# Kernel tuning notes

Hardware: AMD Instinct MI355X
Metric: run time of the kernel (lower is better)

Reference implementation:

```python
import jax, jax.numpy as jnp
import numpy as np

N_HEADS = 16


def setup_inputs() -> dict:
    key = jax.random.key(0)
    k1, k2, k3 = jax.random.split(key, 3)
    B, T, C = 4, 2048, 1024
    x = jax.random.normal(k1, (B, T, C), dtype=jnp.float32)
    # torch nn.Linear weights are (out_features, in_features); y = x @ W.T
    w_in = jax.random.normal(k2, (3 * C, C), dtype=jnp.float32) * 0.02
    w_out = jax.random.normal(k3, (C, C), dtype=jnp.float32) * 0.02
    return {"x": x, "w_in": w_in, "w_out": w_out}


def reference(x, w_in, w_out):
    B, T, C = x.shape
    H = N_HEADS
    hd = C // H

    qkv = x @ w_in.T                      # [B, T, 3C]
    q, k, v = jnp.split(qkv, 3, axis=2)   # each [B, T, C]

    def heads(t):
        return t.reshape(B, T, H, hd).transpose(0, 2, 1, 3)  # [B, H, T, hd]

    q, k, v = heads(q), heads(k), heads(v)

    scale = 1.0 / jnp.sqrt(jnp.float32(hd))
    scores = jnp.einsum('bhqd,bhkd->bhqk', q, k) * scale      # [B, H, T, T]
    causal = jnp.tril(jnp.ones((T, T), dtype=bool))
    scores = jnp.where(causal, scores, -jnp.inf)
    attn = jax.nn.softmax(scores, axis=-1)
    y = jnp.einsum('bhqk,bhkd->bhqd', attn, v)                # [B, H, T, hd]
    y = y.transpose(0, 2, 1, 3).reshape(B, T, C)
    return y @ w_out.T
```

## Files before the change

kernel.cpp:

```cpp
#include <hip/hip_runtime.h>
#include <stdint.h>

#define BB 4
#define TT 2048
#define CC 1024
#define HH 16
#define HD 64
#define C3 3072
#define MM (BB*TT)

typedef __bf16 bf16_t;
typedef bf16_t bf16x8 __attribute__((ext_vector_type(8)));
typedef float f32x4 __attribute__((ext_vector_type(4)));
typedef unsigned short u16;
typedef u16 u16x8 __attribute__((ext_vector_type(8)));
typedef uint32_t u32;

static __device__ __forceinline__ u16 f2bf(float f){
  u32 u = __builtin_bit_cast(u32, f);
  u32 r = (u + 0x7fffu + ((u >> 16) & 1u)) >> 16;
  return (u16)r;
}

static __device__ __forceinline__ f32x4 mfma16(bf16x8 a, bf16x8 b, f32x4 c){
  return __builtin_amdgcn_mfma_f32_16x16x32_bf16(a, b, c, 0, 0, 0);
}

typedef __attribute__((address_space(1))) void* gas_t;
typedef __attribute__((address_space(3))) void* las_t;
static __device__ __forceinline__ void gload16(const void* g, void* l){
  __builtin_amdgcn_global_load_lds((gas_t)g, (las_t)l, 16, 0, 0);
}

__global__ __launch_bounds__(256) void cvt_bf16(const float* __restrict__ in,
                                                u16* __restrict__ out, int n8){
  int stride = gridDim.x * blockDim.x;
  for (int i = blockIdx.x * blockDim.x + threadIdx.x; i < n8; i += stride){
    const float4* p = (const float4*)in + (size_t)i * 2;
    float4 a = p[0], b = p[1];
    u16x8 o;
    o[0]=f2bf(a.x); o[1]=f2bf(a.y); o[2]=f2bf(a.z); o[3]=f2bf(a.w);
    o[4]=f2bf(b.x); o[5]=f2bf(b.y); o[6]=f2bf(b.z); o[7]=f2bf(b.w);
    *((u16x8*)out + i) = o;
  }
}

template<int OUTBF>
__global__ __launch_bounds__(256) void gemm_bt(const u16* __restrict__ A,
                                               const u16* __restrict__ Bm,
                                               void* __restrict__ Cp,
                                               int M, int N, int K){
  __shared__ u16 As[128*32];
  __shared__ u16 Bs[128*32];
  const int tid  = threadIdx.x;
  const int lane = tid & 63;
  const int w    = tid >> 6;
  const int m0   = blockIdx.y * 128;
  const int n0   = blockIdx.x * 128;
  const int wm   = (w >> 1) * 64;
  const int wn   = (w & 1) * 64;
  const int lr   = lane & 15;
  const int lkb  = (lane >> 4) * 16;

  f32x4 acc[4][4] = {};

  const int r0 = w*32 + (lane >> 2);
  const int c8 = (lane & 3) * 8;
  const u16* gA = A  + (size_t)(m0 + r0) * K + c8;
  const u16* gB = Bm + (size_t)(n0 + r0) * K + c8;
  char* lA = (char*)As + w*2048 + lane*16;
  char* lB = (char*)Bs + w*2048 + lane*16;

  for (int k0 = 0; k0 < K; k0 += 32){
    gload16(gA + k0,                 lA);
    gload16(gA + (size_t)16*K + k0,  lA + 1024);
    gload16(gB + k0,                 lB);
    gload16(gB + (size_t)16*K + k0,  lB + 1024);
    __syncthreads();
    bf16x8 af[4], bfr[4];
    #pragma unroll
    for (int m = 0; m < 4; m++)
      af[m] = *(const bf16x8*)((const char*)As + (wm + m*16 + lr)*64 + lkb);
    #pragma unroll
    for (int n = 0; n < 4; n++)
      bfr[n] = *(const bf16x8*)((const char*)Bs + (wn + n*16 + lr)*64 + lkb);
    #pragma unroll
    for (int m = 0; m < 4; m++)
      #pragma unroll
      for (int n = 0; n < 4; n++)
        acc[m][n] = mfma16(af[m], bfr[n], acc[m][n]);
    __syncthreads();
  }

  const int cr = (lane >> 4) * 4;
  #pragma unroll
  for (int m = 0; m < 4; m++)
    #pragma unroll
    for (int n = 0; n < 4; n++)
      #pragma unroll
      for (int j = 0; j < 4; j++){
        size_t row = (size_t)(m0 + wm + m*16 + cr + j);
        size_t col = (size_t)(n0 + wn + n*16 + lr);
        if (OUTBF) ((u16*)Cp)[row*(size_t)N + col] = f2bf(acc[m][n][j]);
        else       ((float*)Cp)[row*(size_t)N + col] = acc[m][n][j];
      }
}

__global__ __launch_bounds__(256, 2) void attn_fwd(const u16* __restrict__ qkv,
                                                   u16* __restrict__ y){
  __shared__ u16 Kl[64*72];
  __shared__ u16 Vt[64*72];
  const int bid = blockIdx.x;
  const int tq = bid >> 6;
  const int h = bid & 15, b = (bid >> 4) & 3;
  const int tid = threadIdx.x, lane = tid & 63, w = tid >> 6;
  const int lr = lane & 15, lg = lane >> 4;
  const size_t base = (size_t)b * TT * C3;
  const int qA = tq*64 + w*16;
  const int qB = (31-tq)*64 + w*16;

  bf16x8 qf[2][2];
  {
    const u16* qp0 = qkv + base + (size_t)(qA + lr) * C3 + h*HD;
    qf[0][0] = *(const bf16x8*)(qp0 + lg*8);
    qf[0][1] = *(const bf16x8*)(qp0 + 32 + lg*8);
    const u16* qp1 = qkv + base + (size_t)(qB + lr) * C3 + h*HD;
    qf[1][0] = *(const bf16x8*)(qp1 + lg*8);
    qf[1][1] = *(const bf16x8*)(qp1 + 32 + lg*8);
  }

  const int rK = tid >> 3, cK = tid & 7;
  const int rV = tid & 31, cV = tid >> 5;
  const u16* gK = qkv + base + (size_t)rK * C3 + CC   + h*HD + cK*8;
  const u16* gV = qkv + base + (size_t)rV * C3 + 2*CC + h*HD + cV*8;

  const int kkey = ((rK >> 3) & 1) << 5;
  const int kw0 = rK*72 + ((cK*8) ^ kkey);
  const int kw1 = (rK+32)*72 + ((cK*8) ^ kkey);

  const int rdx = ((lr >> 2) & 1) << 5;
  const int rbase = 8*(lr >> 2) + (lr & 3);

  u16x8 kreg[2], vreg[2];
  kreg[0] = *(const u16x8*)(gK);
  kreg[1] = *(const u16x8*)(gK + (size_t)32*C3);
  vreg[0] = *(const u16x8*)(gV);
  vreg[1] = *(const u16x8*)(gV + (size_t)32*C3);

  f32x4 o[2][4] = {};
  float mj[2] = {-1e30f, -1e30f};
  float lj[2] = {0.f, 0.f};
  const float SC = 0.18033688011112042f;

  const int ktmax = 31 - tq;
  for (int kt = 0; kt <= ktmax; kt++){
    __syncthreads();
    *(u16x8*)&Kl[kw0] = kreg[0];
    *(u16x8*)&Kl[kw1] = kreg[1];
    #pragma unroll
    for (int i = 0; i < 2; i++)
      #pragma unroll
      for (int e = 0; e < 8; e++)
        Vt[(cV*8+e)*72 + i*32 + rV] = vreg[i][e];
    __syncthreads();

    if (kt < ktmax){
      const u16* gk2 = gK + (size_t)(kt+1)*64*C3;
      const u16* gv2 = gV + (size_t)(kt+1)*64*C3;
      kreg[0] = *(const u16x8*)(gk2);
      kreg[1] = *(const u16x8*)(gk2 + (size_t)32*C3);
      vreg[0] = *(const u16x8*)(gv2);
      vreg[1] = *(const u16x8*)(gv2 + (size_t)32*C3);
    }

    const bool m0act = (kt <= tq);

    f32x4 s[2][4] = {};
    __builtin_amdgcn_s_setprio(1);
    #pragma unroll
    for (int n = 0; n < 4; n++){
      const int rho = 32*(n>>1) + 4*(n&1) + rbase;
      bf16x8 kb0 = *(const bf16x8*)&Kl[rho*72 + ((     lg*8) ^ rdx)];
      bf16x8 kb1 = *(const bf16x8*)&Kl[rho*72 + ((32 + lg*8) ^ rdx)];
      if (m0act){
        s[0][n] = mfma16(kb0, qf[0][0], s[0][n]);
        s[0][n] = mfma16(kb1, qf[0][1], s[0][n]);
      }
      s[1][n] = mfma16(kb0, qf[1][0], s[1][n]);
      s[1][n] = mfma16(kb1, qf[1][1], s[1][n]);
    }
    __builtin_amdgcn_s_setprio(0);

    bf16x8 paA[2], paB[2];
    #pragma unroll
    for (int m = 0; m < 2; m++){
      if (m == 0 && !m0act) continue;
      const int qrow = (m ? qB : qA) + lr;
      const bool dm = (kt == (m ? ktmax : tq));
      float t[4][4];
      #pragma unroll
      for (int n = 0; n < 4; n++)
        #pragma unroll
        for (int j = 0; j < 4; j++){
          float v = s[m][n][j] * SC;
          if (dm && (kt*64 + 32*(n>>1) + 8*lg + 4*(n&1) + j > qrow)) v = -1e30f;
          t[n][j] = v;
        }
      float tm = t[0][0];
      #pragma unroll
      for (int n = 0; n < 4; n++)
        #pragma unroll
        for (int j = 0; j < 4; j++) tm = fmaxf(tm, t[n][j]);
      tm = fmaxf(tm, __shfl_xor(tm, 16, 64));
      tm = fmaxf(tm, __shfl_xor(tm, 32, 64));
      float mo = mj[m];
      if (!__all(tm <= mo)){
        float mn = fmaxf(mo, tm);
        float al = __builtin_amdgcn_exp2f(mo - mn);
        mj[m] = mn;
        lj[m] *= al;
        float a0 = __shfl(al, lg*4+0, 16);
        float a1 = __shfl(al, lg*4+1, 16);
        float a2 = __shfl(al, lg*4+2, 16);
        float a3 = __shfl(al, lg*4+3, 16);
        #pragma unroll
        for (int n = 0; n < 4; n++){
          o[m][n][0] *= a0; o[m][n][1] *= a1;
          o[m][n][2] *= a2; o[m][n][3] *= a3;
        }
      }
      float mm = mj[m];
      float ps = 0.f;
      float p[4][4];
      #pragma unroll
      for (int n = 0; n < 4; n++){
        p[n][0] = __builtin_amdgcn_exp2f(t[n][0] - mm);
        p[n][1] = __builtin_amdgcn_exp2f(t[n][1] - mm);
        p[n][2] = __builtin_amdgcn_exp2f(t[n][2] - mm);
        p[n][3] = __builtin_amdgcn_exp2f(t[n][3] - mm);
        ps += (p[n][0] + p[n][1]) + (p[n][2] + p[n][3]);
      }
      ps += __shfl_xor(ps, 16, 64);
      ps += __shfl_xor(ps, 32, 64);
      lj[m] += ps;
      bf16x8 pa, pb;
      #pragma unroll
      for (int j = 0; j < 4; j++){
        pa[j]   = (bf16_t)p[0][j];
        pa[4+j] = (bf16_t)p[1][j];
        pb[j]   = (bf16_t)p[2][j];
        pb[4+j] = (bf16_t)p[3][j];
      }
      paA[m] = pa; paB[m] = pb;
    }

    __builtin_amdgcn_s_setprio(1);
    #pragma unroll
    for (int n = 0; n < 4; n++){
      bf16x8 vb0 = *(const bf16x8*)&Vt[(n*16+lr)*72 +      lg*8];
      bf16x8 vb1 = *(const bf16x8*)&Vt[(n*16+lr)*72 + 32 + lg*8];
      if (m0act){
        o[0][n] = mfma16(paA[0], vb0, o[0][n]);
        o[0][n] = mfma16(paB[0], vb1, o[0][n]);
      }
      o[1][n] = mfma16(paA[1], vb0, o[1][n]);
      o[1][n] = mfma16(paB[1], vb1, o[1][n]);
    }
    __builtin_amdgcn_s_setprio(0);
  }

  #pragma unroll
  for (int m = 0; m < 2; m++){
    float inv = 1.0f / lj[m];
    float i0 = __shfl(inv, lg*4+0, 16);
    float i1 = __shfl(inv, lg*4+1, 16);
    float i2 = __shfl(inv, lg*4+2, 16);
    float i3 = __shfl(inv, lg*4+3, 16);
    const int qb = (m ? qB : qA);
    #pragma unroll
    for (int j = 0; j < 4; j++){
      float ij = (j==0) ? i0 : (j==1) ? i1 : (j==2) ? i2 : i3;
      size_t row = (size_t)b*TT + qb + lg*4 + j;
      #pragma unroll
      for (int n = 0; n < 4; n++)
        y[row*CC + h*HD + n*16 + lr] = f2bf(o[m][n][j] * ij);
    }
  }
}

extern "C" void kernel_launch(void* const* d_in, const int* in_sizes, int n_in,
                              void* d_out, int out_size, void* d_ws, size_t ws_size,
                              hipStream_t stream){
  const float* x     = (const float*)d_in[0];
  const float* w_in  = (const float*)d_in[1];
  const float* w_out = (const float*)d_in[2];
  float* out = (float*)d_out;

  u16* xb   = (u16*)d_ws;
  u16* wib  = xb  + (size_t)MM * CC;
  u16* wob  = wib + (size_t)C3 * CC;
  u16* qkvb = wob + (size_t)CC * CC;
  u16* yb   = xb;

  auto nblk = [](int n8){ int g = (n8 + 255) / 256; return g > 2048 ? 2048 : g; };
  cvt_bf16<<<nblk(MM*CC/8), 256, 0, stream>>>(x,     xb,  MM*CC/8);
  cvt_bf16<<<nblk(C3*CC/8), 256, 0, stream>>>(w_in,  wib, C3*CC/8);
  cvt_bf16<<<nblk(CC*CC/8), 256, 0, stream>>>(w_out, wob, CC*CC/8);

  gemm_bt<1><<<dim3(C3/128, MM/128), 256, 0, stream>>>(xb, wib, (void*)qkvb, MM, C3, CC);
  attn_fwd<<<1024, 256, 0, stream>>>(qkvb, yb);
  gemm_bt<0><<<dim3(CC/128, MM/128), 256, 0, stream>>>(yb, wob, (void*)out, MM, CC, CC);
}
```

Baseline: 197.3 us.

## Deepen GEMM K-tile with swizzled LDS, remap blocks per XCD, streamline softmax

The GEMM now loads 64-wide K tiles into an XOR-swizzled shared-memory layout, which halves barrier count and reduces LDS bank conflicts. It also remaps the 1D block id so that consecutive tiles land on the same XCD for L2 reuse. In attention, the softmax scale is folded into Q once at load, the mask is applied in place, and the max rescale is skipped unless the new max exceeds the old by more than 4. Occupancy is raised to 3 blocks per SM. Risks include register spills at the higher occupancy, extra Q rounding, and the lazy rescale threshold allowing larger exponent values.

```diff
diff --git a/kernel.cpp b/kernel.cpp
--- a/kernel.cpp
+++ b/kernel.cpp
@@ -49,50 +49,64 @@
 __global__ __launch_bounds__(256) void gemm_bt(const u16* __restrict__ A,
                                                const u16* __restrict__ Bm,
                                                void* __restrict__ Cp,
-                                               int M, int N, int K){
-  __shared__ u16 As[128*32];
-  __shared__ u16 Bs[128*32];
+                                               int M, int N, int K,
+                                               int nbx, int cpx){
+  __shared__ u16 As[128*64];
+  __shared__ u16 Bs[128*64];
+  const int bid = blockIdx.x;
+  const int nb = (bid & 7) * cpx + (bid >> 3);
+  const int by = nb / nbx, bx = nb - by * nbx;
   const int tid  = threadIdx.x;
   const int lane = tid & 63;
   const int w    = tid >> 6;
-  const int m0   = blockIdx.y * 128;
-  const int n0   = blockIdx.x * 128;
+  const int m0   = by * 128;
+  const int n0   = bx * 128;
   const int wm   = (w >> 1) * 64;
   const int wn   = (w & 1) * 64;
   const int lr   = lane & 15;
-  const int lkb  = (lane >> 4) * 16;
+  const int lg4  = lane >> 4;
 
   f32x4 acc[4][4] = {};
 
-  const int r0 = w*32 + (lane >> 2);
-  const int c8 = (lane & 3) * 8;
-  const u16* gA = A  + (size_t)(m0 + r0) * K + c8;
-  const u16* gB = Bm + (size_t)(n0 + r0) * K + c8;
-  char* lA = (char*)As + w*2048 + lane*16;
-  char* lB = (char*)Bs + w*2048 + lane*16;
-
-  for (int k0 = 0; k0 < K; k0 += 32){
-    gload16(gA + k0,                 lA);
-    gload16(gA + (size_t)16*K + k0,  lA + 1024);
-    gload16(gB + k0,                 lB);
-    gload16(gB + (size_t)16*K + k0,  lB + 1024);
+  const int rq  = tid >> 3;
+  const int c8s = ((tid & 7) ^ (rq & 7)) * 8;
+  const u16* gA = A  + (size_t)(m0 + rq) * K + c8s;
+  const u16* gB = Bm + (size_t)(n0 + rq) * K + c8s;
+  char* lA = (char*)As + tid*16;
+  char* lB = (char*)Bs + tid*16;
+
+  for (int k0 = 0; k0 < K; k0 += 64){
+    #pragma unroll
+    for (int q = 0; q < 4; q++){
+      gload16(gA + (size_t)(q*32)*K + k0, lA + q*4096);
+      gload16(gB + (size_t)(q*32)*K + k0, lB + q*4096);
+    }
     __syncthreads();
-    bf16x8 af[4], bfr[4];
-    #pragma unroll
-    for (int m = 0; m < 4; m++)
-      af[m] = *(const bf16x8*)((const char*)As + (wm + m*16 + lr)*64 + lkb);
-    #pragma unroll
-    for (int n = 0; n < 4; n++)
-      bfr[n] = *(const bf16x8*)((const char*)Bs + (wn + n*16 + lr)*64 + lkb);
-    #pragma unroll
-    for (int m = 0; m < 4; m++)
-      #pragma unroll
-      for (int n = 0; n < 4; n++)
-        acc[m][n] = mfma16(af[m], bfr[n], acc[m][n]);
+    #pragma unroll
+    for (int kk = 0; kk < 2; kk++){
+      bf16x8 af[4], bfr[4];
+      #pragma unroll
+      for (int m = 0; m < 4; m++){
+        int row = wm + m*16 + lr;
+        int slot = ((kk<<2) | lg4) ^ (row & 7);
+        af[m] = *(const bf16x8*)((const char*)As + row*128 + slot*16);
+      }
+      #pragma unroll
+      for (int n = 0; n < 4; n++){
+        int row = wn + n*16 + lr;
+        int slot = ((kk<<2) | lg4) ^ (row & 7);
+        bfr[n] = *(const bf16x8*)((const char*)Bs + row*128 + slot*16);
+      }
+      #pragma unroll
+      for (int m = 0; m < 4; m++)
+        #pragma unroll
+        for (int n = 0; n < 4; n++)
+          acc[m][n] = mfma16(af[m], bfr[n], acc[m][n]);
+    }
     __syncthreads();
   }
 
-  const int cr = (lane >> 4) * 4;
+  const int cr = lg4 * 4;
   #pragma unroll
   for (int m = 0; m < 4; m++)
     #pragma unroll
@@ -106,7 +120,7 @@
       }
 }
 
-__global__ __launch_bounds__(256, 2) void attn_fwd(const u16* __restrict__ qkv,
+__global__ __launch_bounds__(256, 3) void attn_fwd(const u16* __restrict__ qkv,
                                                    u16* __restrict__ y){
   __shared__ u16 Kl[64*72];
   __shared__ u16 Vt[64*72];
@@ -118,6 +132,7 @@
   const size_t base = (size_t)b * TT * C3;
   const int qA = tq*64 + w*16;
   const int qB = (31-tq)*64 + w*16;
+  const float SC = 0.18033688011112042f;
 
   bf16x8 qf[2][2];
   {
@@ -127,6 +142,13 @@
     const u16* qp1 = qkv + base + (size_t)(qB + lr) * C3 + h*HD;
     qf[1][0] = *(const bf16x8*)(qp1 + lg*8);
     qf[1][1] = *(const bf16x8*)(qp1 + 32 + lg*8);
+    #pragma unroll
+    for (int m = 0; m < 2; m++)
+      #pragma unroll
+      for (int i = 0; i < 2; i++)
+        #pragma unroll
+        for (int e = 0; e < 8; e++)
+          qf[m][i][e] = (bf16_t)((float)qf[m][i][e] * SC);
   }
 
   const int rK = tid >> 3, cK = tid & 7;
@@ -150,7 +172,6 @@
   f32x4 o[2][4] = {};
   float mj[2] = {-1e30f, -1e30f};
   float lj[2] = {0.f, 0.f};
-  const float SC = 0.18033688011112042f;
 
   const int ktmax = 31 - tq;
   for (int kt = 0; kt <= ktmax; kt++){
@@ -197,24 +218,23 @@
       if (m == 0 && !m0act) continue;
       const int qrow = (m ? qB : qA) + lr;
       const bool dm = (kt == (m ? ktmax : tq));
-      float t[4][4];
+      if (dm){
+        #pragma unroll
+        for (int n = 0; n < 4; n++)
+          #pragma unroll
+          for (int j = 0; j < 4; j++)
+            if (kt*64 + 32*(n>>1) + 8*lg + 4*(n&1) + j > qrow)
+              s[m][n][j] = -1e30f;
+      }
+      float tm = s[m][0][0];
       #pragma unroll
       for (int n = 0; n < 4; n++)
         #pragma unroll
-        for (int j = 0; j < 4; j++){
-          float v = s[m][n][j] * SC;
-          if (dm && (kt*64 + 32*(n>>1) + 8*lg + 4*(n&1) + j > qrow)) v = -1e30f;
-          t[n][j] = v;
-        }
-      float tm = t[0][0];
-      #pragma unroll
-      for (int n = 0; n < 4; n++)
-        #pragma unroll
-        for (int j = 0; j < 4; j++) tm = fmaxf(tm, t[n][j]);
+        for (int j = 0; j < 4; j++) tm = fmaxf(tm, s[m][n][j]);
       tm = fmaxf(tm, __shfl_xor(tm, 16, 64));
       tm = fmaxf(tm, __shfl_xor(tm, 32, 64));
       float mo = mj[m];
-      if (!__all(tm <= mo)){
+      if (!__all(tm <= mo + 4.0f)){
         float mn = fmaxf(mo, tm);
         float al = __builtin_amdgcn_exp2f(mo - mn);
         mj[m] = mn;
@@ -231,26 +251,22 @@
       }
       float mm = mj[m];
       float ps = 0.f;
-      float p[4][4];
+      bf16x8 pa, pb;
       #pragma unroll
       for (int n = 0; n < 4; n++){
-        p[n][0] = __builtin_amdgcn_exp2f(t[n][0] - mm);
-        p[n][1] = __builtin_amdgcn_exp2f(t[n][1] - mm);
-        p[n][2] = __builtin_amdgcn_exp2f(t[n][2] - mm);
-        p[n][3] = __builtin_amdgcn_exp2f(t[n][3] - mm);
-        ps += (p[n][0] + p[n][1]) + (p[n][2] + p[n][3]);
+        float p0 = __builtin_amdgcn_exp2f(s[m][n][0] - mm);
+        float p1 = __builtin_amdgcn_exp2f(s[m][n][1] - mm);
+        float p2 = __builtin_amdgcn_exp2f(s[m][n][2] - mm);
+        float p3 = __builtin_amdgcn_exp2f(s[m][n][3] - mm);
+        ps += (p0 + p1) + (p2 + p3);
+        if (n == 0){ pa[0]=(bf16_t)p0; pa[1]=(bf16_t)p1; pa[2]=(bf16_t)p2; pa[3]=(bf16_t)p3; }
+        if (n == 1){ pa[4]=(bf16_t)p0; pa[5]=(bf16_t)p1; pa[6]=(bf16_t)p2; pa[7]=(bf16_t)p3; }
+        if (n == 2){ pb[0]=(bf16_t)p0; pb[1]=(bf16_t)p1; pb[2]=(bf16_t)p2; pb[3]=(bf16_t)p3; }
+        if (n == 3){ pb[4]=(bf16_t)p0; pb[5]=(bf16_t)p1; pb[6]=(bf16_t)p2; pb[7]=(bf16_t)p3; }
       }
       ps += __shfl_xor(ps, 16, 64);
       ps += __shfl_xor(ps, 32, 64);
       lj[m] += ps;
-      bf16x8 pa, pb;
-      #pragma unroll
-      for (int j = 0; j < 4; j++){
-        pa[j]   = (bf16_t)p[0][j];
-        pa[4+j] = (bf16_t)p[1][j];
-        pb[j]   = (bf16_t)p[2][j];
-        pb[4+j] = (bf16_t)p[3][j];
-      }
       paA[m] = pa; paB[m] = pb;
     }
 
@@ -307,7 +323,7 @@
   cvt_bf16<<<nblk(C3*CC/8), 256, 0, stream>>>(w_in,  wib, C3*CC/8);
   cvt_bf16<<<nblk(CC*CC/8), 256, 0, stream>>>(w_out, wob, CC*CC/8);
 
-  gemm_bt<1><<<dim3(C3/128, MM/128), 256, 0, stream>>>(xb, wib, (void*)qkvb, MM, C3, CC);
+  gemm_bt<1><<<1536, 256, 0, stream>>>(xb, wib, (void*)qkvb, MM, C3, CC, 24, 192);
   attn_fwd<<<1024, 256, 0, stream>>>(qkvb, yb);
-  gemm_bt<0><<<dim3(CC/128, MM/128), 256, 0, stream>>>(yb, wob, (void*)out, MM, CC, CC);
-}
+  gemm_bt<0><<<512, 256, 0, stream>>>(yb, wob, (void*)out, MM, CC, CC, 8, 64);
+}
```

After: 172.7 us. -12.5%, faster.
